# Performance work log

Hardware: AMD Instinct MI355X
Metric: run time of the kernel (lower is better)

The kernel has to match this reference:

```python
import math
import jax, jax.numpy as jnp
import numpy as np
from math import factorial as fact

RS_IN = [(8, 0), (8, 1)]
RS_OUT = [(8, 0), (8, 1)]
N_PATH = 384
HIDDEN = 64
B, N_OUT_PTS, N_IN_PTS = 2, 256, 256

def _lfilters(l_in, l_out, lmax=10):
    return [l for l in range(abs(l_in - l_out), l_in + l_out + 1) if l <= lmax]

# ---- Clebsch-Gordan / Wigner-3j in the real spherical-harmonic basis ----
def _cg(j1, m1, j2, m2, j3, m3):
    if m1 + m2 != m3:
        return 0.0
    kmin = max(0, j2 - j3 - m1, j1 - j3 + m2)
    kmax = min(j1 + j2 - j3, j1 - m1, j2 + m2)
    if kmax < kmin:
        return 0.0
    pre = math.sqrt((2 * j3 + 1) * fact(j3 + j1 - j2) * fact(j3 - j1 + j2) * fact(j1 + j2 - j3) / fact(j1 + j2 + j3 + 1))
    pre *= math.sqrt(fact(j3 + m3) * fact(j3 - m3) * fact(j1 - m1) * fact(j1 + m1) * fact(j2 - m2) * fact(j2 + m2))
    s = sum((-1) ** k / (fact(k) * fact(j1 + j2 - j3 - k) * fact(j1 - m1 - k) * fact(j2 + m2 - k) * fact(j3 - j2 + m1 + k) * fact(j3 - j1 - m2 + k)) for k in range(kmin, kmax + 1))
    return pre * s

def _wigner3j(j1, j2, j3):
    W = np.zeros((2 * j1 + 1, 2 * j2 + 1, 2 * j3 + 1))
    for m1 in range(-j1, j1 + 1):
        for m2 in range(-j2, j2 + 1):
            m3 = -(m1 + m2)
            if abs(m3) <= j3:
                W[m1 + j1, m2 + j2, m3 + j3] = (-1) ** (j1 - j2 - m3) / math.sqrt(2 * j3 + 1) * _cg(j1, m1, j2, m2, j3, -m3)
    return W

def _A(l):
    # change of basis real<->complex SH: Y^real_a = sum_m A[a, m] Y^complex_m
    A = np.zeros((2 * l + 1, 2 * l + 1), dtype=np.complex128)
    A[l, l] = 1.0
    for m in range(1, l + 1):
        A[l + m, l + m] = (-1) ** m / math.sqrt(2)
        A[l + m, l - m] = 1.0 / math.sqrt(2)
        A[l - m, l - m] = 1j / math.sqrt(2)
        A[l - m, l + m] = -1j * (-1) ** m / math.sqrt(2)
    return A

def _real_cg(l1, l2, l3):
    W = _wigner3j(l1, l2, l3).astype(np.complex128)
    Q = np.einsum('am,bn,cp,mnp->abc', _A(l1).conj(), _A(l2).conj(), _A(l3).conj(), W)
    v = Q.flat[int(np.argmax(np.abs(Q)))]
    if abs(v) > 1e-12:
        Q = Q * (v.conjugate() / abs(v))  # rotate global phase so tensor is real
    assert np.abs(Q.imag).max() < 1e-8
    return Q.real.astype(np.float32)

# ---- real spherical harmonics of unit directions, l = 0, 1, 2 ----
_C0 = 0.28209479177387814
_C1 = 0.4886025119029199
_C2A = 1.0925484305920792
_C2B = 0.31539156525252005
_C2C = 0.5462742152960396

def _sh(xyz):
    r = jnp.linalg.norm(xyz, axis=-1, keepdims=True)
    u = xyz / jnp.maximum(r, 1e-12)
    x, y, z = u[..., 0], u[..., 1], u[..., 2]
    Y0 = _C0 * jnp.ones_like(x)[..., None]
    Y1 = _C1 * jnp.stack([y, z, x], axis=-1)
    Y2 = jnp.stack([_C2A * x * y, _C2A * y * z, _C2B * (3.0 * z * z - 1.0), _C2A * x * z, _C2C * (x * x - y * y)], axis=-1)
    return {0: Y0, 1: Y1, 2: Y2}


def setup_inputs() -> dict:
    key = jax.random.key(0)
    ks = jax.random.split(key, 3)
    dm = jax.random.normal(ks[0], (B, N_OUT_PTS, N_IN_PTS, 3), dtype=jnp.float32)
    W1 = 0.1 * jax.random.normal(ks[1], (1, HIDDEN), dtype=jnp.float32)
    b1 = jnp.zeros((HIDDEN,), dtype=jnp.float32)
    W2 = (1.0 / math.sqrt(HIDDEN)) * jax.random.normal(ks[2], (HIDDEN, N_PATH), dtype=jnp.float32)
    b2 = jnp.zeros((N_PATH,), dtype=jnp.float32)
    Q00 = jnp.asarray(_real_cg(0, 0, 0))  # (1,1,1)
    Q01 = jnp.asarray(_real_cg(0, 1, 1))  # (1,3,3)
    Q10 = jnp.asarray(_real_cg(1, 0, 1))  # (3,1,3)
    Q11 = jnp.asarray(np.concatenate([_real_cg(1, 1, l) for l in (0, 1, 2)], axis=2))  # (3,3,9)
    return {"difference_matrix": dm, "W1": W1, "b1": b1, "W2": W2, "b2": b2, "Q00": Q00, "Q01": Q01, "Q10": Q10, "Q11": Q11}


def reference(difference_matrix, W1, b1, W2, b2, Q00, Q01, Q10, Q11):
    Bb, No, Ni, _ = difference_matrix.shape
    Ys = _sh(difference_matrix)                       # l -> [B, No, Ni, 2l+1]
    radii = jnp.linalg.norm(difference_matrix, axis=-1)
    h = jax.nn.relu(radii[..., None] * W1[0] + b1)    # radial MLP
    weights = h @ W2 + b2                             # [B, No, Ni, N_PATH]
    Qs = {(0, 0): Q00, (0, 1): Q01, (1, 0): Q10, (1, 1): Q11}
    begin_w = 0
    rows = []
    for i, (mul_out, l_out) in enumerate(RS_OUT):
        num = sum(mul_in * len(_lfilters(l_in, l_out)) for mul_in, l_in in RS_IN) * Ni
        cols = []
        for j, (mul_in, l_in) in enumerate(RS_IN):
            lfs = _lfilters(l_in, l_out)
            n = mul_out * mul_in * len(lfs)
            w = weights[..., begin_w:begin_w + n].reshape(Bb, No, Ni, mul_out, mul_in, len(lfs))
            begin_w += n
            Q = Qs[(i, j)]
            K = 0.0
            off = 0
            for k, lf in enumerate(lfs):
                Qk = Q[:, :, off:off + 2 * lf + 1]
                off += 2 * lf + 1
                # i=m_out, j=m_in, r=m_filter, b n m = batch/N_out/N_in, u v = mul_out/mul_in
                K = K + jnp.einsum('ijr,bnmr,bnmuv->uivjbnm', Qk, Ys[lf], w[..., k])
            K = K * (math.sqrt(2 * l_in + 1) * math.sqrt(4.0 * math.pi) / math.sqrt(num))
            cols.append(K.reshape(mul_out * (2 * l_out + 1), mul_in * (2 * l_in + 1), Bb, No, Ni))
        rows.append(jnp.concatenate(cols, axis=1))
    return jnp.concatenate(rows, axis=0)  # [n_out, n_in, B, N_out, N_in]
```

## Files before the change

kernel.cpp:

```cpp
#include <hip/hip_runtime.h>
#include <math.h>

namespace {

typedef float f32x4 __attribute__((ext_vector_type(4)));

constexpr int kPts  = 2 * 256 * 256;
constexpr int kHid  = 64;
constexpr int kPath = 384;

constexpr size_t kWsNeedBytes = (kPath + 1) * sizeof(float);

constexpr float kY0   = 0.28209479177387814f;
constexpr float kC1   = 0.4886025119029199f;
constexpr float kC2A  = 1.0925484305920792f;
constexpr float kC2B  = 0.31539156525252005f;
constexpr float kC2C  = 0.5462742152960396f;
constexpr float kS4pi = 3.5449077018110318f;
constexpr float kSq3  = 1.7320508075688772f;
constexpr float kN00  = kS4pi / 64.f;
constexpr float kN01  = kSq3 * kS4pi / 64.f;
constexpr float kN10  = kS4pi / 90.50966799187809f;
constexpr float kN11  = kSq3 * kS4pi / 90.50966799187809f;

__global__ void prep_kernel(const float* __restrict__ W1,
                            const float* __restrict__ b1,
                            const float* __restrict__ W2,
                            float* __restrict__ V,
                            unsigned* __restrict__ flag)
{
    int t = blockIdx.x * 256 + threadIdx.x;
    if (t < kPath) {
        float acc = 0.f;
        for (int i = 0; i < kHid; ++i)
            acc += fmaxf(W1[i], 0.f) * W2[i * kPath + t];
        V[t] = acc;
    }
    if (t == 0) {
        unsigned f = 1u;
        for (int i = 0; i < kHid; ++i)
            if (b1[i] != 0.f) f = 0u;
        *flag = f;
    }
}

__global__ __launch_bounds__(256)
void plane_kernel(const float* __restrict__ dm,
                  const float* __restrict__ W1,
                  const float* __restrict__ b1,
                  const float* __restrict__ W2,
                  const float* __restrict__ b2,
                  const float* __restrict__ Q00,
                  const float* __restrict__ Q01,
                  const float* __restrict__ Q10,
                  const float* __restrict__ Q11,
                  const float* __restrict__ V,
                  const unsigned* __restrict__ flag,
                  float* __restrict__ out)
{
    const int uv = blockIdx.y, u = uv >> 3, v = uv & 7;
    const size_t base = (size_t)blockIdx.x * 2048 + threadIdx.x;

    float R[8], X[8], Y[8], Z[8];
#pragma unroll
    for (int k = 0; k < 8; ++k) {
        size_t pt = base + 256 * (size_t)k;
        float dx = dm[3 * pt], dy = dm[3 * pt + 1], dz = dm[3 * pt + 2];
        float r  = sqrtf(dx * dx + dy * dy + dz * dz);
        float inv = 1.f / fmaxf(r, 1e-12f);
        R[k] = r; X[k] = dx * inv; Y[k] = dy * inv; Z[k] = dz * inv;
    }

    const int pw[6] = { uv, 64 + uv, 128 + uv,
                        192 + 3 * uv, 193 + 3 * uv, 194 + 3 * uv };
    float w[6][8];
    if (*flag != 0u) {
#pragma unroll
        for (int c = 0; c < 6; ++c) {
            float vc = V[pw[c]], bc = b2[pw[c]];
#pragma unroll
            for (int k = 0; k < 8; ++k) w[c][k] = fmaf(R[k], vc, bc);
        }
    } else {
#pragma unroll
        for (int c = 0; c < 6; ++c) {
            float bc = b2[pw[c]];
#pragma unroll
            for (int k = 0; k < 8; ++k) w[c][k] = bc;
        }
#pragma unroll 1
        for (int i = 0; i < kHid; ++i) {
            float w1i = W1[i], b1i = b1[i];
            const float* row = W2 + (size_t)i * kPath;
            float cr[6];
#pragma unroll
            for (int c = 0; c < 6; ++c) cr[c] = row[pw[c]];
#pragma unroll
            for (int k = 0; k < 8; ++k) {
                float h = fmaxf(fmaf(R[k], w1i, b1i), 0.f);
#pragma unroll
                for (int c = 0; c < 6; ++c) w[c][k] = fmaf(h, cr[c], w[c][k]);
            }
        }
    }

    float* __restrict__ oseg = out + base;

    {
        float s00p = kN00 * Q00[0] * kY0;
        float* o = oseg + (size_t)(u * 32 + v) * kPts;
#pragma unroll
        for (int k = 0; k < 8; ++k) o[256 * k] = s00p * w[0][k];
    }
#pragma unroll 1
    for (int jc = 0; jc < 3; ++jc) {
        float a0 = kN01 * kC1 * Q01[jc * 3 + 0];
        float a1 = kN01 * kC1 * Q01[jc * 3 + 1];
        float a2 = kN01 * kC1 * Q01[jc * 3 + 2];
        float* o = oseg + (size_t)(u * 32 + 8 + v * 3 + jc) * kPts;
#pragma unroll
        for (int k = 0; k < 8; ++k) {
            float g = fmaf(a2, X[k], fmaf(a1, Z[k], a0 * Y[k]));
            o[256 * k] = g * w[1][k];
        }
    }
#pragma unroll 1
    for (int ir = 0; ir < 3; ++ir) {
        float a0 = kN10 * kC1 * Q10[ir * 3 + 0];
        float a1 = kN10 * kC1 * Q10[ir * 3 + 1];
        float a2 = kN10 * kC1 * Q10[ir * 3 + 2];
        float* o = oseg + (size_t)((8 + u * 3 + ir) * 32 + v) * kPts;
#pragma unroll
        for (int k = 0; k < 8; ++k) {
            float g = fmaf(a2, X[k], fmaf(a1, Z[k], a0 * Y[k]));
            o[256 * k] = g * w[2][k];
        }
    }
#pragma unroll 1
    for (int e = 0; e < 9; ++e) {
        const float* q = Q11 + e * 9;
        float g0 = kN11 * kY0 * q[0];
        float a0 = kN11 * kC1 * q[1];
        float a1 = kN11 * kC1 * q[2];
        float a2 = kN11 * kC1 * q[3];
        float b0 = kN11 * kC2A * q[4];
        float b1c = kN11 * kC2A * q[5];
        float b2c = kN11 * kC2B * q[6];
        float b3 = kN11 * kC2A * q[7];
        float b4 = kN11 * kC2C * q[8];
        float* o = oseg + (size_t)((8 + u * 3 + e / 3) * 32 + 8 + v * 3 + e % 3) * kPts;
#pragma unroll
        for (int k = 0; k < 8; ++k) {
            float lin = fmaf(a2, X[k], fmaf(a1, Z[k], a0 * Y[k]));
            float zz  = fmaf(3.f * Z[k], Z[k], -1.f);
            float quad = fmaf(b0, X[k] * Y[k],
                         fmaf(b1c, Y[k] * Z[k],
                         fmaf(b2c, zz,
                         fmaf(b3, X[k] * Z[k],
                              b4 * fmaf(X[k], X[k], -(Y[k] * Y[k]))))));
            o[256 * k] = fmaf(g0, w[3][k], fmaf(lin, w[4][k], quad * w[5][k]));
        }
    }
}

__global__ __launch_bounds__(256)
void mono_kernel(const float* __restrict__ dm,
                 const float* __restrict__ W1,
                 const float* __restrict__ b1,
                 const float* __restrict__ W2,
                 const float* __restrict__ b2,
                 const float* __restrict__ Q00,
                 const float* __restrict__ Q01,
                 const float* __restrict__ Q10,
                 const float* __restrict__ Q11,
                 float* __restrict__ out)
{
    const int g   = blockIdx.x * blockDim.x + threadIdx.x;
    const int uv0 = blockIdx.y * 8;

    const f32x4* dmv = reinterpret_cast<const f32x4*>(dm) + 3 * (size_t)g;
    f32x4 f0 = dmv[0], f1 = dmv[1], f2 = dmv[2];
    float px[4] = { f0.x, f0.w, f1.z, f2.y };
    float py[4] = { f0.y, f1.x, f1.w, f2.z };
    float pz[4] = { f0.z, f1.y, f2.x, f2.w };

    float r[4], ux[4], uy[4], uz[4];
#pragma unroll
    for (int p = 0; p < 4; ++p) {
        r[p] = sqrtf(px[p]*px[p] + py[p]*py[p] + pz[p]*pz[p]);
        float inv = 1.0f / fmaxf(r[p], 1e-12f);
        ux[p] = px[p]*inv; uy[p] = py[p]*inv; uz[p] = pz[p]*inv;
    }
    float Y10[4], Y11v[4], Y12[4], Y2[5][4];
#pragma unroll
    for (int p = 0; p < 4; ++p) {
        Y10[p] = kC1 * uy[p]; Y11v[p] = kC1 * uz[p]; Y12[p] = kC1 * ux[p];
        Y2[0][p] = kC2A * ux[p] * uy[p];
        Y2[1][p] = kC2A * uy[p] * uz[p];
        Y2[2][p] = kC2B * (3.f * uz[p] * uz[p] - 1.f);
        Y2[3][p] = kC2A * ux[p] * uz[p];
        Y2[4][p] = kC2C * (ux[p]*ux[p] - uy[p]*uy[p]);
    }
    const float s00 = kN00 * Q00[0] * kY0;
    float G0[9];
#pragma unroll
    for (int e = 0; e < 9; ++e) G0[e] = kN11 * Q11[e*9] * kY0;
    float g01[3][4], g10[3][4], G1[9][4], G2[9][4];
#pragma unroll
    for (int jc = 0; jc < 3; ++jc)
#pragma unroll
        for (int p = 0; p < 4; ++p)
            g01[jc][p] = kN01 * (Q01[jc*3]*Y10[p] + Q01[jc*3+1]*Y11v[p] + Q01[jc*3+2]*Y12[p]);
#pragma unroll
    for (int ir = 0; ir < 3; ++ir)
#pragma unroll
        for (int p = 0; p < 4; ++p)
            g10[ir][p] = kN10 * (Q10[ir*3]*Y10[p] + Q10[ir*3+1]*Y11v[p] + Q10[ir*3+2]*Y12[p]);
#pragma unroll
    for (int e = 0; e < 9; ++e) {
        const float* q = Q11 + e * 9;
#pragma unroll
        for (int p = 0; p < 4; ++p) {
            G1[e][p] = kN11 * (q[1]*Y10[p] + q[2]*Y11v[p] + q[3]*Y12[p]);
            G2[e][p] = kN11 * (q[4]*Y2[0][p] + q[5]*Y2[1][p] + q[6]*Y2[2][p] +
                               q[7]*Y2[3][p] + q[8]*Y2[4][p]);
        }
    }
    float* __restrict__ obase = out + 4 * (size_t)g;
    auto stf = [&](int row, const float* v4) {
        f32x4 q; q.x=v4[0]; q.y=v4[1]; q.z=v4[2]; q.w=v4[3];
        *reinterpret_cast<f32x4*>(obase + (size_t)row * kPts) = q;
    };
#pragma unroll 1
    for (int t = 0; t < 8; ++t) {
        const int uv = uv0 + t;
        float a00[4], a01v[4], a10v[4], a110[4], a111[4], a112[4];
#pragma unroll
        for (int p = 0; p < 4; ++p) {
            a00[p]=b2[uv]; a01v[p]=b2[64+uv]; a10v[p]=b2[128+uv];
            a110[p]=b2[192+3*uv]; a111[p]=b2[193+3*uv]; a112[p]=b2[194+3*uv];
        }
#pragma unroll 1
        for (int i = 0; i < kHid; ++i) {
            float w1i = W1[i], b1i = b1[i];
            const float* row = W2 + (size_t)i * kPath;
            float c00=row[uv], c01=row[64+uv], c10=row[128+uv];
            float c50=row[192+3*uv], c51=row[193+3*uv], c52=row[194+3*uv];
#pragma unroll
            for (int p = 0; p < 4; ++p) {
                float hi = fmaxf(fmaf(r[p], w1i, b1i), 0.f);
                a00[p]=fmaf(hi,c00,a00[p]); a01v[p]=fmaf(hi,c01,a01v[p]);
                a10v[p]=fmaf(hi,c10,a10v[p]); a110[p]=fmaf(hi,c50,a110[p]);
                a111[p]=fmaf(hi,c51,a111[p]); a112[p]=fmaf(hi,c52,a112[p]);
            }
        }
        const int u = uv >> 3, v = uv & 7;
        const int rowu = u * 32;
        float tmp[4];
#pragma unroll
        for (int p = 0; p < 4; ++p) tmp[p] = s00 * a00[p];
        stf(rowu + v, tmp);
#pragma unroll
        for (int jc = 0; jc < 3; ++jc) {
#pragma unroll
            for (int p = 0; p < 4; ++p) tmp[p] = g01[jc][p] * a01v[p];
            stf(rowu + 8 + v*3 + jc, tmp);
        }
#pragma unroll
        for (int ir = 0; ir < 3; ++ir) {
            const int rowb = (8 + u*3 + ir) * 32;
#pragma unroll
            for (int p = 0; p < 4; ++p) tmp[p] = g10[ir][p] * a10v[p];
            stf(rowb + v, tmp);
#pragma unroll
            for (int jc = 0; jc < 3; ++jc) {
                const int e = ir*3 + jc;
#pragma unroll
                for (int p = 0; p < 4; ++p)
                    tmp[p] = fmaf(G0[e], a110[p], fmaf(G1[e][p], a111[p], G2[e][p]*a112[p]));
                stf(rowb + 8 + v*3 + jc, tmp);
            }
        }
    }
}

}

extern "C" void kernel_launch(void* const* d_in, const int* in_sizes, int n_in,
                              void* d_out, int out_size, void* d_ws, size_t ws_size,
                              hipStream_t stream)
{
    const float* dm  = (const float*)d_in[0];
    const float* W1  = (const float*)d_in[1];
    const float* b1  = (const float*)d_in[2];
    const float* W2  = (const float*)d_in[3];
    const float* b2  = (const float*)d_in[4];
    const float* Q00 = (const float*)d_in[5];
    const float* Q01 = (const float*)d_in[6];
    const float* Q10 = (const float*)d_in[7];
    const float* Q11 = (const float*)d_in[8];
    float* out = (float*)d_out;

    if (ws_size >= kWsNeedBytes) {
        float*    V    = (float*)d_ws;
        unsigned* flag = (unsigned*)(V + kPath);
        prep_kernel<<<2, 256, 0, stream>>>(W1, b1, W2, V, flag);
        plane_kernel<<<dim3(kPts / 2048, 64), 256, 0, stream>>>(
            dm, W1, b1, W2, b2, Q00, Q01, Q10, Q11, V, flag, out);
    } else {
        mono_kernel<<<dim3(kPts / 4 / 256, 8), 256, 0, stream>>>(
            dm, W1, b1, W2, b2, Q00, Q01, Q10, Q11, out);
    }
}
```

Baseline: 112.0 us.

## Stage per-point radius/direction, write output rows with vectorized float4 stores

A staging kernel computes radius and unit direction once per point into workspace, alongside the collapsed first-layer weights V and the zero-bias flag. A new row kernel then gives each 1024-thread block four output rows, precomputes the per-row coefficients once, and streams all points with float4 stores. The intent is to cut the repeated per-(u,v) direction recomputation and the scalar strided stores of the old plane kernel. The cost is an extra workspace round trip and one more launch, and the non-zero-bias case now goes through the old mono kernel.

```diff
diff --git a/kernel.cpp b/kernel.cpp
--- a/kernel.cpp
+++ b/kernel.cpp
@@ -9,7 +9,9 @@
 constexpr int kHid  = 64;
 constexpr int kPath = 384;
 
-constexpr size_t kWsNeedBytes = (kPath + 1) * sizeof(float);
+constexpr size_t kVOff    = (size_t)kPts * 4;
+constexpr size_t kFlagOff = kVOff + kPath;
+constexpr size_t kNeedBytes = (kFlagOff + 1) * sizeof(float);
 
 constexpr float kY0   = 0.28209479177387814f;
 constexpr float kC1   = 0.4886025119029199f;
@@ -23,146 +25,144 @@
 constexpr float kN10  = kS4pi / 90.50966799187809f;
 constexpr float kN11  = kSq3 * kS4pi / 90.50966799187809f;
 
-__global__ void prep_kernel(const float* __restrict__ W1,
-                            const float* __restrict__ b1,
-                            const float* __restrict__ W2,
-                            float* __restrict__ V,
-                            unsigned* __restrict__ flag)
-{
-    int t = blockIdx.x * 256 + threadIdx.x;
-    if (t < kPath) {
-        float acc = 0.f;
-        for (int i = 0; i < kHid; ++i)
-            acc += fmaxf(W1[i], 0.f) * W2[i * kPath + t];
-        V[t] = acc;
-    }
-    if (t == 0) {
-        unsigned f = 1u;
-        for (int i = 0; i < kHid; ++i)
-            if (b1[i] != 0.f) f = 0u;
-        *flag = f;
-    }
-}
-
 __global__ __launch_bounds__(256)
-void plane_kernel(const float* __restrict__ dm,
+void stage_kernel(const float* __restrict__ dm,
                   const float* __restrict__ W1,
                   const float* __restrict__ b1,
                   const float* __restrict__ W2,
-                  const float* __restrict__ b2,
-                  const float* __restrict__ Q00,
-                  const float* __restrict__ Q01,
-                  const float* __restrict__ Q10,
-                  const float* __restrict__ Q11,
-                  const float* __restrict__ V,
-                  const unsigned* __restrict__ flag,
-                  float* __restrict__ out)
+                  f32x4* __restrict__ ru,
+                  float* __restrict__ V,
+                  unsigned* __restrict__ flag)
 {
-    const int uv = blockIdx.y, u = uv >> 3, v = uv & 7;
-    const size_t base = (size_t)blockIdx.x * 2048 + threadIdx.x;
-
-    float R[8], X[8], Y[8], Z[8];
-#pragma unroll
-    for (int k = 0; k < 8; ++k) {
-        size_t pt = base + 256 * (size_t)k;
-        float dx = dm[3 * pt], dy = dm[3 * pt + 1], dz = dm[3 * pt + 2];
-        float r  = sqrtf(dx * dx + dy * dy + dz * dz);
-        float inv = 1.f / fmaxf(r, 1e-12f);
-        R[k] = r; X[k] = dx * inv; Y[k] = dy * inv; Z[k] = dz * inv;
-    }
-
-    const int pw[6] = { uv, 64 + uv, 128 + uv,
-                        192 + 3 * uv, 193 + 3 * uv, 194 + 3 * uv };
-    float w[6][8];
-    if (*flag != 0u) {
-#pragma unroll
-        for (int c = 0; c < 6; ++c) {
-            float vc = V[pw[c]], bc = b2[pw[c]];
-#pragma unroll
-            for (int k = 0; k < 8; ++k) w[c][k] = fmaf(R[k], vc, bc);
-        }
-    } else {
-#pragma unroll
-        for (int c = 0; c < 6; ++c) {
-            float bc = b2[pw[c]];
-#pragma unroll
-            for (int k = 0; k < 8; ++k) w[c][k] = bc;
-        }
+    const int pt = blockIdx.x * 256 + threadIdx.x;
+    float dx = dm[3 * pt], dy = dm[3 * pt + 1], dz = dm[3 * pt + 2];
+    float r  = sqrtf(dx * dx + dy * dy + dz * dz);
+    float inv = 1.f / fmaxf(r, 1e-12f);
+    f32x4 q; q.x = r; q.y = dx * inv; q.z = dy * inv; q.w = dz * inv;
+    ru[pt] = q;
+
+    if (blockIdx.x == 0) {
+        for (int p = threadIdx.x; p < kPath; p += 256) {
+            float acc = 0.f;
+            for (int i = 0; i < kHid; ++i)
+                acc += fmaxf(W1[i], 0.f) * W2[i * kPath + p];
+            V[p] = acc;
+        }
+        if (threadIdx.x == 0) {
+            unsigned f = 1u;
+            for (int i = 0; i < kHid; ++i)
+                if (b1[i] != 0.f) f = 0u;
+            *flag = f;
+        }
+    }
+}
+
+__global__ __launch_bounds__(1024)
+void row_kernel(const f32x4* __restrict__ ru,
+                const float* __restrict__ V,
+                const float* __restrict__ b2,
+                const float* __restrict__ Q00,
+                const float* __restrict__ Q01,
+                const float* __restrict__ Q10,
+                const float* __restrict__ Q11,
+                const unsigned* __restrict__ flag,
+                float* __restrict__ out)
+{
+    if (*flag == 0u) return;
+    const int tid = threadIdx.x;
+
+    float P0[4], A0[4], A1[4], A2[4], B0[4], B1[4], B2v[4], B3[4], B4[4];
+    float VX[4], CX[4], VY[4], CY[4], VZ[4], CZ[4];
+#pragma unroll
+    for (int j = 0; j < 4; ++j) {
+        const int row = blockIdx.x * 4 + j;
+        const int rA = row >> 5, rB = row & 31;
+        float p0=0, a0=0, a1=0, a2=0, b0=0, b1v=0, b2c=0, b3=0, b4=0;
+        float vx=0, cx=0, vy=0, cy=0, vz=0, cz=0;
+        if (rA < 8) {
+            const int u = rA;
+            if (rB < 8) {
+                const int uv = u * 8 + rB;
+                p0 = kN00 * Q00[0] * kY0;
+                vx = V[uv]; cx = b2[uv];
+            } else {
+                const int v = (rB - 8) / 3, jc = (rB - 8) % 3, uv = u * 8 + v;
+                a0 = kN01 * kC1 * Q01[jc * 3 + 0];
+                a1 = kN01 * kC1 * Q01[jc * 3 + 1];
+                a2 = kN01 * kC1 * Q01[jc * 3 + 2];
+                vy = V[64 + uv]; cy = b2[64 + uv];
+            }
+        } else {
+            const int t = rA - 8, u = t / 3, ir = t % 3;
+            if (rB < 8) {
+                const int uv = u * 8 + rB;
+                a0 = kN10 * kC1 * Q10[ir * 3 + 0];
+                a1 = kN10 * kC1 * Q10[ir * 3 + 1];
+                a2 = kN10 * kC1 * Q10[ir * 3 + 2];
+                vy = V[128 + uv]; cy = b2[128 + uv];
+            } else {
+                const int v = (rB - 8) / 3, jc = (rB - 8) % 3;
+                const int e = ir * 3 + jc, uv = u * 8 + v;
+                const float* q = Q11 + e * 9;
+                p0 = kN11 * kY0 * q[0];
+                vx = V[192 + 3 * uv]; cx = b2[192 + 3 * uv];
+                a0 = kN11 * kC1 * q[1];
+                a1 = kN11 * kC1 * q[2];
+                a2 = kN11 * kC1 * q[3];
+                vy = V[193 + 3 * uv]; cy = b2[193 + 3 * uv];
+                b0  = kN11 * kC2A * q[4];
+                b1v = kN11 * kC2A * q[5];
+                b2c = kN11 * kC2B * q[6];
+                b3  = kN11 * kC2A * q[7];
+                b4  = kN11 * kC2C * q[8];
+                vz = V[194 + 3 * uv]; cz = b2[194 + 3 * uv];
+            }
+        }
+        P0[j]=p0; A0[j]=a0; A1[j]=a1; A2[j]=a2;
+        B0[j]=b0; B1[j]=b1v; B2v[j]=b2c; B3[j]=b3; B4[j]=b4;
+        VX[j]=vx; CX[j]=cx; VY[j]=vy; CY[j]=cy; VZ[j]=vz; CZ[j]=cz;
+    }
+
+    const size_t rowbase = (size_t)blockIdx.x * 4 * kPts;
+
 #pragma unroll 1
-        for (int i = 0; i < kHid; ++i) {
-            float w1i = W1[i], b1i = b1[i];
-            const float* row = W2 + (size_t)i * kPath;
-            float cr[6];
-#pragma unroll
-            for (int c = 0; c < 6; ++c) cr[c] = row[pw[c]];
-#pragma unroll
-            for (int k = 0; k < 8; ++k) {
-                float h = fmaxf(fmaf(R[k], w1i, b1i), 0.f);
-#pragma unroll
-                for (int c = 0; c < 6; ++c) w[c][k] = fmaf(h, cr[c], w[c][k]);
-            }
-        }
-    }
-
-    float* __restrict__ oseg = out + base;
-
-    {
-        float s00p = kN00 * Q00[0] * kY0;
-        float* o = oseg + (size_t)(u * 32 + v) * kPts;
-#pragma unroll
-        for (int k = 0; k < 8; ++k) o[256 * k] = s00p * w[0][k];
-    }
-#pragma unroll 1
-    for (int jc = 0; jc < 3; ++jc) {
-        float a0 = kN01 * kC1 * Q01[jc * 3 + 0];
-        float a1 = kN01 * kC1 * Q01[jc * 3 + 1];
-        float a2 = kN01 * kC1 * Q01[jc * 3 + 2];
-        float* o = oseg + (size_t)(u * 32 + 8 + v * 3 + jc) * kPts;
-#pragma unroll
-        for (int k = 0; k < 8; ++k) {
-            float g = fmaf(a2, X[k], fmaf(a1, Z[k], a0 * Y[k]));
-            o[256 * k] = g * w[1][k];
-        }
-    }
-#pragma unroll 1
-    for (int ir = 0; ir < 3; ++ir) {
-        float a0 = kN10 * kC1 * Q10[ir * 3 + 0];
-        float a1 = kN10 * kC1 * Q10[ir * 3 + 1];
-        float a2 = kN10 * kC1 * Q10[ir * 3 + 2];
-        float* o = oseg + (size_t)((8 + u * 3 + ir) * 32 + v) * kPts;
-#pragma unroll
-        for (int k = 0; k < 8; ++k) {
-            float g = fmaf(a2, X[k], fmaf(a1, Z[k], a0 * Y[k]));
-            o[256 * k] = g * w[2][k];
-        }
-    }
-#pragma unroll 1
-    for (int e = 0; e < 9; ++e) {
-        const float* q = Q11 + e * 9;
-        float g0 = kN11 * kY0 * q[0];
-        float a0 = kN11 * kC1 * q[1];
-        float a1 = kN11 * kC1 * q[2];
-        float a2 = kN11 * kC1 * q[3];
-        float b0 = kN11 * kC2A * q[4];
-        float b1c = kN11 * kC2A * q[5];
-        float b2c = kN11 * kC2B * q[6];
-        float b3 = kN11 * kC2A * q[7];
-        float b4 = kN11 * kC2C * q[8];
-        float* o = oseg + (size_t)((8 + u * 3 + e / 3) * 32 + 8 + v * 3 + e % 3) * kPts;
-#pragma unroll
-        for (int k = 0; k < 8; ++k) {
-            float lin = fmaf(a2, X[k], fmaf(a1, Z[k], a0 * Y[k]));
-            float zz  = fmaf(3.f * Z[k], Z[k], -1.f);
-            float quad = fmaf(b0, X[k] * Y[k],
-                         fmaf(b1c, Y[k] * Z[k],
-                         fmaf(b2c, zz,
-                         fmaf(b3, X[k] * Z[k],
-                              b4 * fmaf(X[k], X[k], -(Y[k] * Y[k]))))));
-            o[256 * k] = fmaf(g0, w[3][k], fmaf(lin, w[4][k], quad * w[5][k]));
-        }
-    }
-}
-
+    for (int c = 0; c < kPts / 4096; ++c) {
+        const int pt0 = c * 4096 + tid * 4;
+        f32x4 q0 = ru[pt0], q1 = ru[pt0 + 1], q2 = ru[pt0 + 2], q3 = ru[pt0 + 3];
+        float R[4] = { q0.x, q1.x, q2.x, q3.x };
+        float X[4] = { q0.y, q1.y, q2.y, q3.y };
+        float Y[4] = { q0.z, q1.z, q2.z, q3.z };
+        float Z[4] = { q0.w, q1.w, q2.w, q3.w };
+        float XY[4], YZ[4], ZZ[4], XZ[4], XXYY[4];
+#pragma unroll
+        for (int k = 0; k < 4; ++k) {
+            XY[k] = X[k] * Y[k];
+            YZ[k] = Y[k] * Z[k];
+            ZZ[k] = fmaf(3.f * Z[k], Z[k], -1.f);
+            XZ[k] = X[k] * Z[k];
+            XXYY[k] = fmaf(X[k], X[k], -(Y[k] * Y[k]));
+        }
+#pragma unroll
+        for (int j = 0; j < 4; ++j) {
+            f32x4 o;
+#pragma unroll
+            for (int k = 0; k < 4; ++k) {
+                float wx = fmaf(R[k], VX[j], CX[j]);
+                float wy = fmaf(R[k], VY[j], CY[j]);
+                float wz = fmaf(R[k], VZ[j], CZ[j]);
+                float lin = fmaf(A2[j], X[k], fmaf(A1[j], Z[k], A0[j] * Y[k]));
+                float quad = fmaf(B0[j], XY[k],
+                             fmaf(B1[j], YZ[k],
+                             fmaf(B2v[j], ZZ[k],
+                             fmaf(B3[j], XZ[k], B4[j] * XXYY[k]))));
+                o[k] = fmaf(P0[j], wx, fmaf(lin, wy, quad * wz));
+            }
+            *reinterpret_cast<f32x4*>(out + rowbase + (size_t)j * kPts + pt0) = o;
+        }
+    }
+}
+
+template <bool PRED>
 __global__ __launch_bounds__(256)
 void mono_kernel(const float* __restrict__ dm,
                  const float* __restrict__ W1,
@@ -173,8 +173,10 @@
                  const float* __restrict__ Q01,
                  const float* __restrict__ Q10,
                  const float* __restrict__ Q11,
+                 const unsigned* __restrict__ flag,
                  float* __restrict__ out)
 {
+    if constexpr (PRED) { if (*flag != 0u) return; }
     const int g   = blockIdx.x * blockDim.x + threadIdx.x;
     const int uv0 = blockIdx.y * 8;
 
@@ -301,14 +303,18 @@
     const float* Q11 = (const float*)d_in[8];
     float* out = (float*)d_out;
 
-    if (ws_size >= kWsNeedBytes) {
-        float*    V    = (float*)d_ws;
-        unsigned* flag = (unsigned*)(V + kPath);
-        prep_kernel<<<2, 256, 0, stream>>>(W1, b1, W2, V, flag);
-        plane_kernel<<<dim3(kPts / 2048, 64), 256, 0, stream>>>(
-            dm, W1, b1, W2, b2, Q00, Q01, Q10, Q11, V, flag, out);
+    if (ws_size >= kNeedBytes) {
+        float*    ws   = (float*)d_ws;
+        f32x4*    ru   = (f32x4*)ws;
+        float*    V    = ws + kVOff;
+        unsigned* flag = (unsigned*)(ws + kFlagOff);
+        stage_kernel<<<kPts / 256, 256, 0, stream>>>(dm, W1, b1, W2, ru, V, flag);
+        mono_kernel<true><<<dim3(kPts / 4 / 256, 8), 256, 0, stream>>>(
+            dm, W1, b1, W2, b2, Q00, Q01, Q10, Q11, flag, out);
+        row_kernel<<<256, 1024, 0, stream>>>(
+            ru, V, b2, Q00, Q01, Q10, Q11, flag, out);
     } else {
-        mono_kernel<<<dim3(kPts / 4 / 256, 8), 256, 0, stream>>>(
-            dm, W1, b1, W2, b2, Q00, Q01, Q10, Q11, out);
-    }
-}
+        mono_kernel<false><<<dim3(kPts / 4 / 256, 8), 256, 0, stream>>>(
+            dm, W1, b1, W2, b2, Q00, Q01, Q10, Q11, nullptr, out);
+    }
+}
```

Result: slower. 259.5 us (+131.8%).
